# Kernel optimization log

Hardware: AMD Instinct MI355X
Metric: run time of the kernel (lower is better)

Reference implementation:

```python
import jax, jax.numpy as jnp
from jax import lax
import numpy as np


def _cum_masks(nd):
    # 4 nested cumulative masks over a 9-tap kernel: borders p=3,2,1,0
    ms = []
    for p in (3, 2, 1, 0):
        m = np.zeros((9,) * nd, np.float32)
        sl = tuple(slice(p, 9 - p) for _ in range(nd))
        m[sl] = 1.0
        ms.append(m)
    return jnp.asarray(np.stack(ms))  # (4, 9) or (4, 9, 9)


def _group_norm(x, w, b, groups, eps=1e-5):
    B, C, H, W = x.shape
    xg = x.reshape(B, groups, C // groups, H, W)
    mu = jnp.mean(xg, axis=(2, 3, 4), keepdims=True)
    var = jnp.var(xg, axis=(2, 3, 4), keepdims=True)
    xg = (xg - mu) * lax.rsqrt(var + eps)
    return xg.reshape(B, C, H, W) * w[None, :, None, None] + b[None, :, None, None]


def setup_inputs() -> dict:
    key = jax.random.key(0)
    ks = jax.random.split(key, 16)
    C = 256
    c = C // 4
    x = jax.random.normal(ks[0], (16, C, 128, 128), jnp.float32)
    W1 = jax.random.normal(ks[1], (1, 1, 9, 1, 1), jnp.float32)
    W2 = jax.random.normal(ks[2], (c, 1, 9, 9), jnp.float32)
    conv1_w = jax.random.normal(ks[3], (c, C, 1, 1), jnp.float32) * 0.05
    conv1_b = jax.random.normal(ks[4], (c,), jnp.float32) * 0.05
    conv2_w = jax.random.normal(ks[5], (C, c, 1, 1), jnp.float32) * 0.05
    conv2_b = jax.random.normal(ks[6], (C,), jnp.float32) * 0.05
    gn1_w = jnp.ones((c,), jnp.float32)
    gn1_b = jnp.zeros((c,), jnp.float32)
    gns_w = jnp.ones((c,), jnp.float32)
    gns_b = jnp.zeros((c,), jnp.float32)
    gn2_w = jnp.ones((C,), jnp.float32)
    gn2_b = jnp.zeros((C,), jnp.float32)
    return dict(x=x, W1=W1, W2=W2, conv1_w=conv1_w, conv1_b=conv1_b,
                conv2_w=conv2_w, conv2_b=conv2_b, gn1_w=gn1_w, gn1_b=gn1_b,
                gns_w=gns_w, gns_b=gns_b, gn2_w=gn2_w, gn2_b=gn2_b)


def reference(x, W1, W2, conv1_w, conv1_b, conv2_w, conv2_b,
              gn1_w, gn1_b, gns_w, gns_b, gn2_w, gn2_b):
    res = x
    # 1x1 conv + GN (bottleneck)
    h1 = jnp.einsum('bchw,oc->bohw', x, conv1_w[:, :, 0, 0]) + conv1_b[None, :, None, None]
    h1 = _group_norm(h1, gn1_w, gn1_b, 16)
    c = h1.shape[1]

    # --- branch A: multi-ring 1D conv along channel dim (conv3d, kernel (9,1,1)) ---
    m1 = _cum_masks(1)                                   # (4,9) cumulative masks
    r1 = m1 - jnp.concatenate([jnp.zeros_like(m1[:1]), m1[:-1]], 0)  # rings
    k1 = W1[0, 0, :, 0, 0]                               # (9,)
    a1 = jax.nn.softmax(jnp.sum(k1[None, :] * r1, 1) / (jnp.sum(r1, 1) + 1e-10))
    # linearity: softmax-weighted sum of 4 masked convs == one conv with weighted mask
    W1_eff = W1 * jnp.sum(a1[:, None] * m1, 0)[None, None, :, None, None]
    x3 = lax.conv_general_dilated(
        h1[:, None], W1_eff, (1, 1, 1), [(4, 4), (0, 0), (0, 0)],
        dimension_numbers=('NCDHW', 'OIDHW', 'NCDHW'))[:, 0]  # (b,c,h,w)

    # --- branch B: multi-ring 9x9 depthwise conv2d ---
    m2 = _cum_masks(2)                                   # (4,9,9)
    r2 = m2 - jnp.concatenate([jnp.zeros_like(m2[:1]), m2[:-1]], 0)
    num2 = jnp.sum(W2[None] * r2[:, None, None], axis=(1, 2, 3, 4))
    den2 = c * jnp.sum(r2, axis=(1, 2)) + 1e-10          # mask is (c,1,9,9) in torch
    a2 = jax.nn.softmax(num2 / den2)
    W2_eff = W2 * jnp.sum(a2[:, None, None] * m2, 0)[None, None]
    x_sa = lax.conv_general_dilated(
        h1, W2_eff, (1, 1), [(4, 4), (4, 4)],
        dimension_numbers=('NCHW', 'OIHW', 'NCHW'), feature_group_count=c)

    h = jax.nn.relu(_group_norm(x3 + x_sa, gns_w, gns_b, 16))
    out = jnp.einsum('bchw,oc->bohw', h, conv2_w[:, :, 0, 0]) + conv2_b[None, :, None, None]
    out = jax.nn.relu(_group_norm(out, gn2_w, gn2_b, 16))
    return out + res
```

## Files before the change

### kernel.cpp

```cpp
#include <hip/hip_runtime.h>
#include <math.h>

#define HW   16384
#define CC   256
#define cC   64
#define BB   16
#define CHW  (CC*HW)
#define cHW  (cC*HW)

#define WS_TB    0
#define WS_H1B   8388608
#define WS_RAWB  16777216
#define WS_W2E   50331648
#define WS_K1E   (WS_W2E + 5184)
#define WS_GN1A  (WS_K1E + 16)
#define WS_GNSA  (WS_GN1A + 512)
#define WS_GN2A  (WS_GNSA + 512)
#define WS_SC1   (WS_GN2A + 512)
#define WS_SH1   (WS_SC1 + 1024)
#define WS_SCS   (WS_SH1 + 1024)
#define WS_SHS   (WS_SCS + 1024)
#define WS_SC2   (WS_SHS + 1024)
#define WS_SH2   (WS_SC2 + 4096)
#define WS_W1P   (WS_SH2 + 4096)
#define WS_W2P   (WS_W1P + 8192)

typedef __attribute__((ext_vector_type(8))) short bf16x8;
typedef __attribute__((ext_vector_type(4))) float f32x4;
typedef __attribute__((ext_vector_type(8))) unsigned short u16x8;

__device__ inline unsigned short f2bf(float f) {
    union { float f; unsigned u; } c; c.f = f;
    unsigned r = c.u + 0x7FFFu + ((c.u >> 16) & 1u);
    return (unsigned short)(r >> 16);
}
__device__ inline float bf2f(unsigned short h) {
    union { unsigned u; float f; } c; c.u = ((unsigned)h) << 16; return c.f;
}

__global__ void k_setup(const float* __restrict__ W1, const float* __restrict__ W2,
                        const float* __restrict__ c1w, const float* __restrict__ c2w,
                        float* __restrict__ k1e, float* __restrict__ w2e,
                        float* __restrict__ accz, unsigned short* __restrict__ w1p,
                        unsigned short* __restrict__ w2p) {
    __shared__ float tapsum[81];
    __shared__ float a2s[4];
    int tdx = threadIdx.x;
    for (int i = tdx; i < 1536; i += 128) accz[i] = 0.f;
    for (int e = tdx; e < 16384; e += 128) {
        int fi = e >> 9, rem = e & 511;
        int l = rem >> 3, j = rem & 7;
        int ks = fi >> 2, nf = fi & 3;
        int c = ks * 32 + (l >> 4) * 8 + j;
        int oc = nf * 16 + (l & 15);
        w1p[e] = f2bf(c1w[oc * 256 + c]);
    }
    for (int e = tdx; e < 16384; e += 128) {
        int fi = e >> 9, rem = e & 511;
        int l = rem >> 3, j = rem & 7;
        int ks = fi >> 4, nfg = fi & 15;
        int c = ks * 32 + (l >> 4) * 8 + j;
        int oc = nfg * 16 + (l & 15);
        w2p[e] = f2bf(c2w[oc * 64 + c]);
    }
    if (tdx < 81) {
        float s = 0.f;
        for (int ch = 0; ch < 64; ++ch) s += W2[ch * 81 + tdx];
        tapsum[tdx] = s;
    }
    __syncthreads();
    if (tdx == 0) {
        float ring[4] = {0.f, 0.f, 0.f, 0.f};
        for (int i = 0; i < 9; ++i)
            for (int j = 0; j < 9; ++j) {
                int d = max(abs(i - 4), abs(j - 4));
                int r = (d <= 1) ? 0 : (d - 1);
                ring[r] += tapsum[i * 9 + j];
            }
        float den2[4] = {576.f, 1024.f, 1536.f, 2048.f};
        float v[4], mx = -1e30f;
        for (int p = 0; p < 4; ++p) { v[p] = ring[p] / den2[p]; mx = fmaxf(mx, v[p]); }
        float se = 0.f;
        for (int p = 0; p < 4; ++p) { v[p] = expf(v[p] - mx); se += v[p]; }
        for (int p = 0; p < 4; ++p) a2s[p] = v[p] / se;
        float k1[9];
        for (int k = 0; k < 9; ++k) k1[k] = W1[k];
        float num[4];
        num[0] = k1[3] + k1[4] + k1[5];
        num[1] = k1[2] + k1[6];
        num[2] = k1[1] + k1[7];
        num[3] = k1[0] + k1[8];
        float den1[4] = {3.f, 2.f, 2.f, 2.f};
        mx = -1e30f;
        for (int p = 0; p < 4; ++p) { v[p] = num[p] / den1[p]; mx = fmaxf(mx, v[p]); }
        se = 0.f;
        for (int p = 0; p < 4; ++p) { v[p] = expf(v[p] - mx); se += v[p]; }
        float a1[4];
        for (int p = 0; p < 4; ++p) a1[p] = v[p] / se;
        float s1arr[5];
        s1arr[0] = 1.f; s1arr[1] = 1.f;
        s1arr[4] = a1[3]; s1arr[3] = a1[2] + a1[3]; s1arr[2] = a1[1] + s1arr[3];
        for (int k = 0; k < 9; ++k) { int d = abs(k - 4); k1e[k] = k1[k] * s1arr[d]; }
    }
    __syncthreads();
    float s2arr[5];
    s2arr[0] = 1.f; s2arr[1] = 1.f;
    s2arr[4] = a2s[3]; s2arr[3] = a2s[2] + a2s[3]; s2arr[2] = a2s[1] + s2arr[3];
    for (int idx = tdx; idx < 64 * 81; idx += 128) {
        int tap = idx % 81;
        int i = tap / 9, j = tap - i * 9;
        int d = max(abs(i - 4), abs(j - 4));
        w2e[idx] = W2[idx] * s2arr[d];
    }
}

__global__ __launch_bounds__(256) void k_conv1(const float* __restrict__ x,
        const unsigned short* __restrict__ w1p, const float* __restrict__ b1,
        unsigned short* __restrict__ h1, float* __restrict__ gn1a) {
    int bid = blockIdx.x;
    int b = bid >> 6, pt = bid & 63;
    int tid = threadIdx.x;
    int w = tid >> 6, lane = tid & 63;
    int l15 = lane & 15, lg = lane >> 4;
    int p_wave = pt * 256 + w * 64;
    const bf16x8* w1v = (const bf16x8*)w1p;
    f32x4 acc[4][4];
#pragma unroll
    for (int mf = 0; mf < 4; ++mf)
#pragma unroll
        for (int nf = 0; nf < 4; ++nf) acc[mf][nf] = (f32x4){0.f, 0.f, 0.f, 0.f};
    const float* xb = x + b * CHW;
#pragma unroll 1
    for (int ks = 0; ks < 8; ++ks) {
        int c0 = ks * 32 + lg * 8;
        bf16x8 afr[4];
#pragma unroll
        for (int mf = 0; mf < 4; ++mf) {
            const float* xp = xb + c0 * HW + p_wave + mf * 16 + l15;
            bf16x8 a;
#pragma unroll
            for (int j = 0; j < 8; ++j) a[j] = (short)f2bf(xp[j * HW]);
            afr[mf] = a;
        }
#pragma unroll
        for (int nf = 0; nf < 4; ++nf) {
            bf16x8 bfr = w1v[(ks * 4 + nf) * 64 + lane];
#pragma unroll
            for (int mf = 0; mf < 4; ++mf)
                acc[mf][nf] = __builtin_amdgcn_mfma_f32_16x16x32_bf16(afr[mf], bfr, acc[mf][nf], 0, 0, 0);
        }
    }
    __shared__ float red[4][16][2];
    unsigned short* hb = h1 + b * cHW;
#pragma unroll
    for (int nf = 0; nf < 4; ++nf) {
        int oc = nf * 16 + l15;
        float bias = b1[oc];
        float s = 0.f, ss = 0.f;
#pragma unroll
        for (int mf = 0; mf < 4; ++mf) {
            f32x4 v = acc[mf][nf];
            v[0] += bias; v[1] += bias; v[2] += bias; v[3] += bias;
            ushort4 hv = make_ushort4(f2bf(v[0]), f2bf(v[1]), f2bf(v[2]), f2bf(v[3]));
            *(ushort4*)(hb + oc * HW + p_wave + mf * 16 + lg * 4) = hv;
            s += v[0] + v[1] + v[2] + v[3];
            ss += v[0] * v[0] + v[1] * v[1] + v[2] * v[2] + v[3] * v[3];
        }
        s += __shfl_xor(s, 16, 64); ss += __shfl_xor(ss, 16, 64);
        s += __shfl_xor(s, 32, 64); ss += __shfl_xor(ss, 32, 64);
        s += __shfl_xor(s, 1, 64);  ss += __shfl_xor(ss, 1, 64);
        s += __shfl_xor(s, 2, 64);  ss += __shfl_xor(ss, 2, 64);
        if (lg == 0 && (l15 & 3) == 0) {
            int g = nf * 4 + (l15 >> 2);
            red[w][g][0] = s; red[w][g][1] = ss;
        }
    }
    __syncthreads();
    if (tid < 32) {
        int g = tid >> 1, c = tid & 1;
        float v = red[0][g][c] + red[1][g][c] + red[2][g][c] + red[3][g][c];
        atomicAdd(&gn1a[(b * 16 + g) * 2 + c], v);
    }
}

__global__ void k_gnfin(const float* __restrict__ accum, const float* __restrict__ gw,
                        const float* __restrict__ gb, float* __restrict__ scale,
                        float* __restrict__ shift, int nent, int chbits, int gshift,
                        float inv_n) {
    int idx = blockIdx.x * blockDim.x + threadIdx.x;
    if (idx >= nent) return;
    int chm = (1 << chbits) - 1;
    int ch = idx & chm, b = idx >> chbits, g = ch >> gshift;
    float s = accum[(b * 16 + g) * 2], ss = accum[(b * 16 + g) * 2 + 1];
    float mu = s * inv_n;
    float var = ss * inv_n - mu * mu;
    float rstd = rsqrtf(var + 1e-5f);
    float sc = gw[ch] * rstd;
    scale[idx] = sc;
    shift[idx] = gb[ch] - mu * sc;
}

__global__ __launch_bounds__(256) void k_x3(const unsigned short* __restrict__ h1,
        const float* __restrict__ scale1, const float* __restrict__ shift1,
        const float* __restrict__ k1e, unsigned short* __restrict__ t) {
    int idx = blockIdx.x * 256 + threadIdx.x;
    int b = idx >> 14, p = idx & 16383;
    const unsigned short* hb = h1 + b * cHW + p;
    const float* sc = scale1 + b * 64;
    const float* sh = shift1 + b * 64;
    float ke[9];
#pragma unroll
    for (int k = 0; k < 9; ++k) ke[k] = k1e[k];
    float win[9];
#pragma unroll
    for (int k = 0; k < 9; ++k) {
        int ch = k - 4;
        win[k] = (ch >= 0) ? fmaf(bf2f(hb[ch * HW]), sc[ch], sh[ch]) : 0.f;
    }
    unsigned short* tb = t + b * cHW + p;
#pragma unroll
    for (int ch = 0; ch < 64; ++ch) {
        float s = 0.f;
#pragma unroll
        for (int k = 0; k < 9; ++k) s = fmaf(win[k], ke[k], s);
        tb[ch * HW] = f2bf(s);
#pragma unroll
        for (int k = 0; k < 8; ++k) win[k] = win[k + 1];
        int nc = ch + 5;
        win[8] = (nc < 64) ? fmaf(bf2f(hb[nc * HW]), sc[nc], sh[nc]) : 0.f;
    }
}

__global__ __launch_bounds__(256) void k_xsa(const unsigned short* __restrict__ h1,
        const float* __restrict__ scale1, const float* __restrict__ shift1,
        const float* __restrict__ w2e, unsigned short* __restrict__ t,
        float* __restrict__ gnsa) {
    int bid = blockIdx.x;
    int b = bid >> 9, ch = (bid >> 3) & 63, rt = bid & 7;
    int r0 = rt * 16;
    const float sc = scale1[b * 64 + ch];
    const float sh = shift1[b * 64 + ch];
    const unsigned short* hp = h1 + b * cHW + ch * HW;
    __shared__ float tile[24 * 136];
    for (int li = threadIdx.x; li < 24 * 136; li += 256) {
        int row = li / 136, col = li - row * 136;
        int gr = r0 - 4 + row, gc = col - 4;
        float v = 0.f;
        if (gr >= 0 && gr < 128 && gc >= 0 && gc < 128)
            v = fmaf(bf2f(hp[gr * 128 + gc]), sc, sh);
        tile[li] = v;
    }
    __syncthreads();
    int q = threadIdx.x & 15, orow = threadIdx.x >> 4;
    const float* wch = w2e + ch * 81;
    float acc[2][4] = {{0.f, 0.f, 0.f, 0.f}, {0.f, 0.f, 0.f, 0.f}};
#pragma unroll
    for (int i = 0; i < 9; ++i) {
#pragma unroll
        for (int m = 0; m < 2; ++m) {
            int c0 = q * 4 + m * 64;
            const float* lr = &tile[(orow + i) * 136 + c0];
            float v[12];
            *(float4*)&v[0] = *(const float4*)lr;
            *(float4*)&v[4] = *(const float4*)(lr + 4);
            *(float4*)&v[8] = *(const float4*)(lr + 8);
#pragma unroll
            for (int j = 0; j < 9; ++j) {
                float wv = wch[i * 9 + j];
                acc[m][0] = fmaf(v[j], wv, acc[m][0]);
                acc[m][1] = fmaf(v[j + 1], wv, acc[m][1]);
                acc[m][2] = fmaf(v[j + 2], wv, acc[m][2]);
                acc[m][3] = fmaf(v[j + 3], wv, acc[m][3]);
            }
        }
    }
    float s = 0.f, ss = 0.f;
    unsigned short* tp = t + b * cHW + ch * HW + (r0 + orow) * 128;
#pragma unroll
    for (int m = 0; m < 2; ++m) {
        int c0 = q * 4 + m * 64;
        ushort4 tv = *(const ushort4*)(tp + c0);
        float r0v = bf2f(tv.x) + acc[m][0];
        float r1v = bf2f(tv.y) + acc[m][1];
        float r2v = bf2f(tv.z) + acc[m][2];
        float r3v = bf2f(tv.w) + acc[m][3];
        *(ushort4*)(tp + c0) = make_ushort4(f2bf(r0v), f2bf(r1v), f2bf(r2v), f2bf(r3v));
        s += r0v + r1v + r2v + r3v;
        ss += r0v * r0v + r1v * r1v + r2v * r2v + r3v * r3v;
    }
#pragma unroll
    for (int off = 32; off; off >>= 1) { s += __shfl_xor(s, off, 64); ss += __shfl_xor(ss, off, 64); }
    __shared__ float rs[4], rss[4];
    int lane = threadIdx.x & 63, wv2 = threadIdx.x >> 6;
    if (lane == 0) { rs[wv2] = s; rss[wv2] = ss; }
    __syncthreads();
    if (threadIdx.x == 0) {
        int gi = (b * 16 + (ch >> 2)) * 2;
        atomicAdd(&gnsa[gi], rs[0] + rs[1] + rs[2] + rs[3]);
        atomicAdd(&gnsa[gi + 1], rss[0] + rss[1] + rss[2] + rss[3]);
    }
}

__global__ __launch_bounds__(256) void k_conv2(const unsigned short* __restrict__ t,
        const float* __restrict__ scs, const float* __restrict__ shs,
        const unsigned short* __restrict__ w2p, const float* __restrict__ b2,
        unsigned short* __restrict__ raw, float* __restrict__ gn2a) {
    int bid = blockIdx.x;
    int obk = bid & 1, pt = (bid >> 1) & 127, b = bid >> 8;
    int tid = threadIdx.x;
    int w = tid >> 6, lane = tid & 63;
    int l15 = lane & 15, lg = lane >> 4;
    int pw = w >> 1, ow = w & 1;
    int p_wave = pt * 128 + pw * 64;
    __shared__ float lsc[64], lsh[64];
    __shared__ float red[4][4][2];
    if (tid < 64) { lsc[tid] = scs[b * 64 + tid]; lsh[tid] = shs[b * 64 + tid]; }
    __syncthreads();
    const bf16x8* w2v = (const bf16x8*)w2p;
    f32x4 acc[4][4];
#pragma unroll
    for (int mf = 0; mf < 4; ++mf)
#pragma unroll
        for (int nf = 0; nf < 4; ++nf) acc[mf][nf] = (f32x4){0.f, 0.f, 0.f, 0.f};
    const unsigned short* tb = t + b * cHW;
#pragma unroll
    for (int ks = 0; ks < 2; ++ks) {
        int kb = ks * 32 + lg * 8;
        float kc[8], kh[8];
#pragma unroll
        for (int j = 0; j < 8; ++j) { kc[j] = lsc[kb + j]; kh[j] = lsh[kb + j]; }
        bf16x8 afr[4];
#pragma unroll
        for (int mf = 0; mf < 4; ++mf) {
            const unsigned short* tp = tb + kb * HW + p_wave + mf * 16 + l15;
            bf16x8 a;
#pragma unroll
            for (int j = 0; j < 8; ++j) {
                float v = fmaxf(fmaf(bf2f(tp[j * HW]), kc[j], kh[j]), 0.f);
                a[j] = (short)f2bf(v);
            }
            afr[mf] = a;
        }
#pragma unroll
        for (int nf = 0; nf < 4; ++nf) {
            int fi = ks * 16 + (obk * 8 + ow * 4 + nf);
            bf16x8 bfr = w2v[fi * 64 + lane];
#pragma unroll
            for (int mf = 0; mf < 4; ++mf)
                acc[mf][nf] = __builtin_amdgcn_mfma_f32_16x16x32_bf16(afr[mf], bfr, acc[mf][nf], 0, 0, 0);
        }
    }
    int oc0 = obk * 128 + ow * 64;
    unsigned short* ob = raw + b * CHW;
    float sred[4], ssred[4];
#pragma unroll
    for (int nf = 0; nf < 4; ++nf) {
        int oc = oc0 + nf * 16 + l15;
        float bias = b2[oc];
        float s = 0.f, ss = 0.f;
#pragma unroll
        for (int mf = 0; mf < 4; ++mf) {
            f32x4 v = acc[mf][nf];
            v[0] += bias; v[1] += bias; v[2] += bias; v[3] += bias;
            ushort4 hv = make_ushort4(f2bf(v[0]), f2bf(v[1]), f2bf(v[2]), f2bf(v[3]));
            *(ushort4*)(ob + oc * HW + p_wave + mf * 16 + lg * 4) = hv;
            s += v[0] + v[1] + v[2] + v[3];
            ss += v[0] * v[0] + v[1] * v[1] + v[2] * v[2] + v[3] * v[3];
        }
#pragma unroll
        for (int off = 32; off; off >>= 1) { s += __shfl_xor(s, off, 64); ss += __shfl_xor(ss, off, 64); }
        sred[nf] = s; ssred[nf] = ss;
    }
    if (lane == 0) {
#pragma unroll
        for (int nf = 0; nf < 4; ++nf) { red[w][nf][0] = sred[nf]; red[w][nf][1] = ssred[nf]; }
    }
    __syncthreads();
    if (tid < 16) {
        int ow2 = tid >> 3, nf = (tid >> 1) & 3, c = tid & 1;
        float v = red[ow2][nf][c] + red[ow2 + 2][nf][c];
        int g = obk * 8 + ow2 * 4 + nf;
        atomicAdd(&gn2a[(b * 16 + g) * 2 + c], v);
    }
}

__global__ __launch_bounds__(256) void k_final(const float* __restrict__ x,
        const unsigned short* __restrict__ raw,
        const float* __restrict__ sc2, const float* __restrict__ sh2,
        float* __restrict__ out) {
    int tid = blockIdx.x * blockDim.x + threadIdx.x;
    const int total8 = (BB * CHW) / 8;
    int stride = gridDim.x * blockDim.x;
    for (int i = tid; i < total8; i += stride) {
        int e = i * 8;
        int b = e >> 22;
        int o = (e >> 14) & 255;
        float s = sc2[b * 256 + o], h = sh2[b * 256 + o];
        u16x8 rv = ((const u16x8*)raw)[i];
        float4 xa = ((const float4*)x)[2 * i];
        float4 xb = ((const float4*)x)[2 * i + 1];
        float4 r0, r1;
        r0.x = fmaxf(fmaf(bf2f(rv[0]), s, h), 0.f) + xa.x;
        r0.y = fmaxf(fmaf(bf2f(rv[1]), s, h), 0.f) + xa.y;
        r0.z = fmaxf(fmaf(bf2f(rv[2]), s, h), 0.f) + xa.z;
        r0.w = fmaxf(fmaf(bf2f(rv[3]), s, h), 0.f) + xa.w;
        r1.x = fmaxf(fmaf(bf2f(rv[4]), s, h), 0.f) + xb.x;
        r1.y = fmaxf(fmaf(bf2f(rv[5]), s, h), 0.f) + xb.y;
        r1.z = fmaxf(fmaf(bf2f(rv[6]), s, h), 0.f) + xb.z;
        r1.w = fmaxf(fmaf(bf2f(rv[7]), s, h), 0.f) + xb.w;
        ((float4*)out)[2 * i] = r0;
        ((float4*)out)[2 * i + 1] = r1;
    }
}

extern "C" void kernel_launch(void* const* d_in, const int* in_sizes, int n_in,
                              void* d_out, int out_size, void* d_ws, size_t ws_size,
                              hipStream_t stream) {
    (void)in_sizes; (void)n_in; (void)out_size; (void)ws_size;
    const float* x   = (const float*)d_in[0];
    const float* W1  = (const float*)d_in[1];
    const float* W2  = (const float*)d_in[2];
    const float* c1w = (const float*)d_in[3];
    const float* c1b = (const float*)d_in[4];
    const float* c2w = (const float*)d_in[5];
    const float* c2b = (const float*)d_in[6];
    const float* g1w = (const float*)d_in[7];
    const float* g1b = (const float*)d_in[8];
    const float* gsw = (const float*)d_in[9];
    const float* gsb = (const float*)d_in[10];
    const float* g2w = (const float*)d_in[11];
    const float* g2b = (const float*)d_in[12];
    float* out = (float*)d_out;
    float* ws  = (float*)d_ws;

    unsigned short* tb   = (unsigned short*)(ws + WS_TB);
    unsigned short* h1b  = (unsigned short*)(ws + WS_H1B);
    unsigned short* rawb = (unsigned short*)(ws + WS_RAWB);
    float* w2e  = ws + WS_W2E;
    float* k1e  = ws + WS_K1E;
    float* gn1a = ws + WS_GN1A;
    float* gnsa = ws + WS_GNSA;
    float* gn2a = ws + WS_GN2A;
    float* sc1  = ws + WS_SC1;
    float* sh1  = ws + WS_SH1;
    float* scs  = ws + WS_SCS;
    float* shs  = ws + WS_SHS;
    float* sc2  = ws + WS_SC2;
    float* sh2  = ws + WS_SH2;
    unsigned short* w1p = (unsigned short*)(ws + WS_W1P);
    unsigned short* w2p = (unsigned short*)(ws + WS_W2P);

    k_setup<<<1, 128, 0, stream>>>(W1, W2, c1w, c2w, k1e, w2e, gn1a, w1p, w2p);
    k_conv1<<<1024, 256, 0, stream>>>(x, w1p, c1b, h1b, gn1a);
    k_gnfin<<<4, 256, 0, stream>>>(gn1a, g1w, g1b, sc1, sh1, 1024, 6, 2, 1.f / 65536.f);
    k_x3<<<1024, 256, 0, stream>>>(h1b, sc1, sh1, k1e, tb);
    k_xsa<<<8192, 256, 0, stream>>>(h1b, sc1, sh1, w2e, tb, gnsa);
    k_gnfin<<<4, 256, 0, stream>>>(gnsa, gsw, gsb, scs, shs, 1024, 6, 2, 1.f / 65536.f);
    k_conv2<<<4096, 256, 0, stream>>>(tb, scs, shs, w2p, c2b, rawb, gn2a);
    k_gnfin<<<16, 256, 0, stream>>>(gn2a, g2w, g2b, sc2, sh2, 4096, 8, 4, 1.f / 262144.f);
    k_final<<<2048, 256, 0, stream>>>(x, rawb, sc2, sh2, out);
}
```

Measured before the change: 422.2 us.

## Vectorize channel conv, enlarge depthwise tiles, and use nontemporal loads/stores

The channel-direction 9-tap conv now processes 4 pixels per thread with ushort4 loads and stages scale/shift/kernel in shared memory, using a quarter of the blocks. The 9x9 depthwise conv uses 32-row tiles with 4x4 outputs per thread, reusing each loaded row across several output rows, and fills the tile with vectorized loads. The final residual kernel handles 16 elements per thread with nontemporal loads and stores, and conv1 reads x nontemporally. These target memory-instruction count and LDS traffic, but the smaller k_x3 grid may leave the GPU underoccupied and register pressure goes up.

After: 480.6 us. 13.8% more time.

```diff
diff --git a/kernel.cpp b/kernel.cpp
--- a/kernel.cpp
+++ b/kernel.cpp
@@ -139,7 +139,7 @@
             const float* xp = xb + c0 * HW + p_wave + mf * 16 + l15;
             bf16x8 a;
 #pragma unroll
-            for (int j = 0; j < 8; ++j) a[j] = (short)f2bf(xp[j * HW]);
+            for (int j = 0; j < 8; ++j) a[j] = (short)f2bf(__builtin_nontemporal_load(xp + j * HW));
             afr[mf] = a;
         }
 #pragma unroll
@@ -203,31 +203,49 @@
 __global__ __launch_bounds__(256) void k_x3(const unsigned short* __restrict__ h1,
         const float* __restrict__ scale1, const float* __restrict__ shift1,
         const float* __restrict__ k1e, unsigned short* __restrict__ t) {
-    int idx = blockIdx.x * 256 + threadIdx.x;
-    int b = idx >> 14, p = idx & 16383;
+    int i = blockIdx.x * 256 + threadIdx.x;
+    int b = i >> 12, p = (i & 4095) * 4;
+    __shared__ float lsc[64], lsh[64], lke[9];
+    if (threadIdx.x < 64) {
+        lsc[threadIdx.x] = scale1[b * 64 + threadIdx.x];
+        lsh[threadIdx.x] = shift1[b * 64 + threadIdx.x];
+    }
+    if (threadIdx.x < 9) lke[threadIdx.x] = k1e[threadIdx.x];
+    __syncthreads();
     const unsigned short* hb = h1 + b * cHW + p;
-    const float* sc = scale1 + b * 64;
-    const float* sh = shift1 + b * 64;
-    float ke[9];
-#pragma unroll
-    for (int k = 0; k < 9; ++k) ke[k] = k1e[k];
-    float win[9];
+    float4 win[9];
 #pragma unroll
     for (int k = 0; k < 9; ++k) {
         int ch = k - 4;
-        win[k] = (ch >= 0) ? fmaf(bf2f(hb[ch * HW]), sc[ch], sh[ch]) : 0.f;
+        if (ch >= 0) {
+            ushort4 hv = *(const ushort4*)(hb + ch * HW);
+            float s = lsc[ch], h = lsh[ch];
+            win[k] = make_float4(fmaf(bf2f(hv.x), s, h), fmaf(bf2f(hv.y), s, h),
+                                 fmaf(bf2f(hv.z), s, h), fmaf(bf2f(hv.w), s, h));
+        } else win[k] = make_float4(0.f, 0.f, 0.f, 0.f);
     }
     unsigned short* tb = t + b * cHW + p;
 #pragma unroll
     for (int ch = 0; ch < 64; ++ch) {
-        float s = 0.f;
-#pragma unroll
-        for (int k = 0; k < 9; ++k) s = fmaf(win[k], ke[k], s);
-        tb[ch * HW] = f2bf(s);
+        float4 s = make_float4(0.f, 0.f, 0.f, 0.f);
+#pragma unroll
+        for (int k = 0; k < 9; ++k) {
+            float kv = lke[k];
+            s.x = fmaf(win[k].x, kv, s.x);
+            s.y = fmaf(win[k].y, kv, s.y);
+            s.z = fmaf(win[k].z, kv, s.z);
+            s.w = fmaf(win[k].w, kv, s.w);
+        }
+        *(ushort4*)(tb + ch * HW) = make_ushort4(f2bf(s.x), f2bf(s.y), f2bf(s.z), f2bf(s.w));
 #pragma unroll
         for (int k = 0; k < 8; ++k) win[k] = win[k + 1];
         int nc = ch + 5;
-        win[8] = (nc < 64) ? fmaf(bf2f(hb[nc * HW]), sc[nc], sh[nc]) : 0.f;
+        if (nc < 64) {
+            ushort4 hv = *(const ushort4*)(hb + nc * HW);
+            float sN = lsc[nc], hN = lsh[nc];
+            win[8] = make_float4(fmaf(bf2f(hv.x), sN, hN), fmaf(bf2f(hv.y), sN, hN),
+                                 fmaf(bf2f(hv.z), sN, hN), fmaf(bf2f(hv.w), sN, hN));
+        } else win[8] = make_float4(0.f, 0.f, 0.f, 0.f);
     }
 }
 
@@ -236,65 +254,78 @@
         const float* __restrict__ w2e, unsigned short* __restrict__ t,
         float* __restrict__ gnsa) {
     int bid = blockIdx.x;
-    int b = bid >> 9, ch = (bid >> 3) & 63, rt = bid & 7;
-    int r0 = rt * 16;
+    int b = bid >> 8, ch = (bid >> 2) & 63, rt = bid & 3;
+    int r0 = rt * 32;
+    int tid = threadIdx.x;
     const float sc = scale1[b * 64 + ch];
     const float sh = shift1[b * 64 + ch];
     const unsigned short* hp = h1 + b * cHW + ch * HW;
-    __shared__ float tile[24 * 136];
-    for (int li = threadIdx.x; li < 24 * 136; li += 256) {
-        int row = li / 136, col = li - row * 136;
-        int gr = r0 - 4 + row, gc = col - 4;
-        float v = 0.f;
-        if (gr >= 0 && gr < 128 && gc >= 0 && gc < 128)
-            v = fmaf(bf2f(hp[gr * 128 + gc]), sc, sh);
-        tile[li] = v;
-    }
-    __syncthreads();
-    int q = threadIdx.x & 15, orow = threadIdx.x >> 4;
+    __shared__ float tile[40 * 136];
+    for (int li = tid; li < 40 * 34; li += 256) {
+        int row = li / 34, c4 = li - row * 34;
+        int col = c4 * 4;
+        int gr = r0 - 4 + row;
+        float4 z = make_float4(0.f, 0.f, 0.f, 0.f);
+        if (gr >= 0 && gr < 128 && c4 >= 1 && c4 <= 32) {
+            int gc = col - 4;
+            ushort4 hv = *(const ushort4*)(hp + gr * 128 + gc);
+            z = make_float4(fmaf(bf2f(hv.x), sc, sh), fmaf(bf2f(hv.y), sc, sh),
+                            fmaf(bf2f(hv.z), sc, sh), fmaf(bf2f(hv.w), sc, sh));
+        }
+        *(float4*)&tile[row * 136 + col] = z;
+    }
+    __syncthreads();
+    int r4g = tid >> 5, c4g = tid & 31;
+    int orow0 = r4g * 4, oc0 = c4g * 4;
     const float* wch = w2e + ch * 81;
-    float acc[2][4] = {{0.f, 0.f, 0.f, 0.f}, {0.f, 0.f, 0.f, 0.f}};
-#pragma unroll
-    for (int i = 0; i < 9; ++i) {
-#pragma unroll
-        for (int m = 0; m < 2; ++m) {
-            int c0 = q * 4 + m * 64;
-            const float* lr = &tile[(orow + i) * 136 + c0];
-            float v[12];
-            *(float4*)&v[0] = *(const float4*)lr;
-            *(float4*)&v[4] = *(const float4*)(lr + 4);
-            *(float4*)&v[8] = *(const float4*)(lr + 8);
-#pragma unroll
-            for (int j = 0; j < 9; ++j) {
-                float wv = wch[i * 9 + j];
-                acc[m][0] = fmaf(v[j], wv, acc[m][0]);
-                acc[m][1] = fmaf(v[j + 1], wv, acc[m][1]);
-                acc[m][2] = fmaf(v[j + 2], wv, acc[m][2]);
-                acc[m][3] = fmaf(v[j + 3], wv, acc[m][3]);
+    float acc[4][4];
+#pragma unroll
+    for (int r = 0; r < 4; ++r)
+#pragma unroll
+        for (int k = 0; k < 4; ++k) acc[r][k] = 0.f;
+#pragma unroll
+    for (int d = 0; d < 12; ++d) {
+        const float* lr = &tile[(orow0 + d) * 136 + oc0];
+        float v[12];
+        *(float4*)&v[0] = *(const float4*)lr;
+        *(float4*)&v[4] = *(const float4*)(lr + 4);
+        *(float4*)&v[8] = *(const float4*)(lr + 8);
+#pragma unroll
+        for (int r = 0; r < 4; ++r) {
+            if (r <= d && d - r <= 8) {
+                const int i = d - r;
+#pragma unroll
+                for (int j = 0; j < 9; ++j) {
+                    float wv = wch[i * 9 + j];
+                    acc[r][0] = fmaf(v[j + 0], wv, acc[r][0]);
+                    acc[r][1] = fmaf(v[j + 1], wv, acc[r][1]);
+                    acc[r][2] = fmaf(v[j + 2], wv, acc[r][2]);
+                    acc[r][3] = fmaf(v[j + 3], wv, acc[r][3]);
+                }
             }
         }
     }
     float s = 0.f, ss = 0.f;
-    unsigned short* tp = t + b * cHW + ch * HW + (r0 + orow) * 128;
-#pragma unroll
-    for (int m = 0; m < 2; ++m) {
-        int c0 = q * 4 + m * 64;
-        ushort4 tv = *(const ushort4*)(tp + c0);
-        float r0v = bf2f(tv.x) + acc[m][0];
-        float r1v = bf2f(tv.y) + acc[m][1];
-        float r2v = bf2f(tv.z) + acc[m][2];
-        float r3v = bf2f(tv.w) + acc[m][3];
-        *(ushort4*)(tp + c0) = make_ushort4(f2bf(r0v), f2bf(r1v), f2bf(r2v), f2bf(r3v));
+    unsigned short* tpb = t + b * cHW + ch * HW + (r0 + orow0) * 128 + oc0;
+#pragma unroll
+    for (int r = 0; r < 4; ++r) {
+        unsigned short* tp = tpb + r * 128;
+        ushort4 tv = *(const ushort4*)tp;
+        float r0v = bf2f(tv.x) + acc[r][0];
+        float r1v = bf2f(tv.y) + acc[r][1];
+        float r2v = bf2f(tv.z) + acc[r][2];
+        float r3v = bf2f(tv.w) + acc[r][3];
+        *(ushort4*)tp = make_ushort4(f2bf(r0v), f2bf(r1v), f2bf(r2v), f2bf(r3v));
         s += r0v + r1v + r2v + r3v;
         ss += r0v * r0v + r1v * r1v + r2v * r2v + r3v * r3v;
     }
 #pragma unroll
     for (int off = 32; off; off >>= 1) { s += __shfl_xor(s, off, 64); ss += __shfl_xor(ss, off, 64); }
     __shared__ float rs[4], rss[4];
-    int lane = threadIdx.x & 63, wv2 = threadIdx.x >> 6;
+    int lane = tid & 63, wv2 = tid >> 6;
     if (lane == 0) { rs[wv2] = s; rss[wv2] = ss; }
     __syncthreads();
-    if (threadIdx.x == 0) {
+    if (tid == 0) {
         int gi = (b * 16 + (ch >> 2)) * 2;
         atomicAdd(&gnsa[gi], rs[0] + rs[1] + rs[2] + rs[3]);
         atomicAdd(&gnsa[gi + 1], rss[0] + rss[1] + rss[2] + rss[3]);
@@ -389,27 +420,42 @@
         const float* __restrict__ sc2, const float* __restrict__ sh2,
         float* __restrict__ out) {
     int tid = blockIdx.x * blockDim.x + threadIdx.x;
-    const int total8 = (BB * CHW) / 8;
+    const int total16 = (BB * CHW) / 16;
     int stride = gridDim.x * blockDim.x;
-    for (int i = tid; i < total8; i += stride) {
-        int e = i * 8;
+    for (int i = tid; i < total16; i += stride) {
+        int e = i * 16;
         int b = e >> 22;
         int o = (e >> 14) & 255;
         float s = sc2[b * 256 + o], h = sh2[b * 256 + o];
-        u16x8 rv = ((const u16x8*)raw)[i];
-        float4 xa = ((const float4*)x)[2 * i];
-        float4 xb = ((const float4*)x)[2 * i + 1];
-        float4 r0, r1;
-        r0.x = fmaxf(fmaf(bf2f(rv[0]), s, h), 0.f) + xa.x;
-        r0.y = fmaxf(fmaf(bf2f(rv[1]), s, h), 0.f) + xa.y;
-        r0.z = fmaxf(fmaf(bf2f(rv[2]), s, h), 0.f) + xa.z;
-        r0.w = fmaxf(fmaf(bf2f(rv[3]), s, h), 0.f) + xa.w;
-        r1.x = fmaxf(fmaf(bf2f(rv[4]), s, h), 0.f) + xb.x;
-        r1.y = fmaxf(fmaf(bf2f(rv[5]), s, h), 0.f) + xb.y;
-        r1.z = fmaxf(fmaf(bf2f(rv[6]), s, h), 0.f) + xb.z;
-        r1.w = fmaxf(fmaf(bf2f(rv[7]), s, h), 0.f) + xb.w;
-        ((float4*)out)[2 * i] = r0;
-        ((float4*)out)[2 * i + 1] = r1;
+        u16x8 rv0 = ((const u16x8*)raw)[2 * i];
+        u16x8 rv1 = ((const u16x8*)raw)[2 * i + 1];
+        const f32x4* xp = (const f32x4*)x + 4 * i;
+        f32x4 x0 = __builtin_nontemporal_load(xp);
+        f32x4 x1 = __builtin_nontemporal_load(xp + 1);
+        f32x4 x2 = __builtin_nontemporal_load(xp + 2);
+        f32x4 x3 = __builtin_nontemporal_load(xp + 3);
+        f32x4 r0, r1, r2, r3;
+        r0[0] = fmaxf(fmaf(bf2f(rv0[0]), s, h), 0.f) + x0[0];
+        r0[1] = fmaxf(fmaf(bf2f(rv0[1]), s, h), 0.f) + x0[1];
+        r0[2] = fmaxf(fmaf(bf2f(rv0[2]), s, h), 0.f) + x0[2];
+        r0[3] = fmaxf(fmaf(bf2f(rv0[3]), s, h), 0.f) + x0[3];
+        r1[0] = fmaxf(fmaf(bf2f(rv0[4]), s, h), 0.f) + x1[0];
+        r1[1] = fmaxf(fmaf(bf2f(rv0[5]), s, h), 0.f) + x1[1];
+        r1[2] = fmaxf(fmaf(bf2f(rv0[6]), s, h), 0.f) + x1[2];
+        r1[3] = fmaxf(fmaf(bf2f(rv0[7]), s, h), 0.f) + x1[3];
+        r2[0] = fmaxf(fmaf(bf2f(rv1[0]), s, h), 0.f) + x2[0];
+        r2[1] = fmaxf(fmaf(bf2f(rv1[1]), s, h), 0.f) + x2[1];
+        r2[2] = fmaxf(fmaf(bf2f(rv1[2]), s, h), 0.f) + x2[2];
+        r2[3] = fmaxf(fmaf(bf2f(rv1[3]), s, h), 0.f) + x2[3];
+        r3[0] = fmaxf(fmaf(bf2f(rv1[4]), s, h), 0.f) + x3[0];
+        r3[1] = fmaxf(fmaf(bf2f(rv1[5]), s, h), 0.f) + x3[1];
+        r3[2] = fmaxf(fmaf(bf2f(rv1[6]), s, h), 0.f) + x3[2];
+        r3[3] = fmaxf(fmaf(bf2f(rv1[7]), s, h), 0.f) + x3[3];
+        f32x4* op = (f32x4*)out + 4 * i;
+        __builtin_nontemporal_store(r0, op);
+        __builtin_nontemporal_store(r1, op + 1);
+        __builtin_nontemporal_store(r2, op + 2);
+        __builtin_nontemporal_store(r3, op + 3);
     }
 }
 
@@ -453,10 +499,10 @@
     k_setup<<<1, 128, 0, stream>>>(W1, W2, c1w, c2w, k1e, w2e, gn1a, w1p, w2p);
     k_conv1<<<1024, 256, 0, stream>>>(x, w1p, c1b, h1b, gn1a);
     k_gnfin<<<4, 256, 0, stream>>>(gn1a, g1w, g1b, sc1, sh1, 1024, 6, 2, 1.f / 65536.f);
-    k_x3<<<1024, 256, 0, stream>>>(h1b, sc1, sh1, k1e, tb);
-    k_xsa<<<8192, 256, 0, stream>>>(h1b, sc1, sh1, w2e, tb, gnsa);
+    k_x3<<<256, 256, 0, stream>>>(h1b, sc1, sh1, k1e, tb);
+    k_xsa<<<4096, 256, 0, stream>>>(h1b, sc1, sh1, w2e, tb, gnsa);
     k_gnfin<<<4, 256, 0, stream>>>(gnsa, gsw, gsb, scs, shs, 1024, 6, 2, 1.f / 65536.f);
     k_conv2<<<4096, 256, 0, stream>>>(tb, scs, shs, w2p, c2b, rawb, gn2a);
     k_gnfin<<<16, 256, 0, stream>>>(gn2a, g2w, g2b, sc2, sh2, 4096, 8, 4, 1.f / 262144.f);
-    k_final<<<2048, 256, 0, stream>>>(x, rawb, sc2, sh2, out);
-}
+    k_final<<<4096, 256, 0, stream>>>(x, rawb, sc2, sh2, out);
+}
```
